# Kernel tuning notes

Hardware: AMD Instinct MI355X
Metric: run time of the kernel (lower is better)

Reference implementation:

```python
import jax, jax.numpy as jnp
import numpy as np

DIM = 2240; HEADS = 20; HD = 112
B = 1; F = 8; H = 16; W = 28; S = F * H * W; ENC = 300
HID = int(3.0 * DIM)  # 6720
EPS_LN = 1e-6; EPS_RMS = 1e-5


def setup_inputs():
    ks = iter(jax.random.split(jax.random.key(0), 64))
    nrm = lambda shape, s=1.0: jax.random.normal(next(ks), shape, jnp.float32) * s
    wsc = 0.02
    inp = dict(
        hidden_states=nrm((B, S, DIM)),
        encoder_hidden_states=nrm((B, ENC, DIM)),
        timestep=nrm((B, 6 * DIM), 0.1),
        freqs_cos=nrm((1, S, 1, HD)),
        freqs_sin=nrm((1, S, 1, HD)),
        scale_shift_table=nrm((6, DIM), 1.0 / np.sqrt(DIM)),
    )
    for p in ("a1", "a2"):
        inp[p + "_qw"] = nrm((DIM, DIM), wsc); inp[p + "_qb"] = jnp.zeros((DIM,), jnp.float32)
        inp[p + "_kw"] = nrm((DIM, DIM), wsc); inp[p + "_kb"] = jnp.zeros((DIM,), jnp.float32)
        inp[p + "_vw"] = nrm((DIM, DIM), wsc); inp[p + "_vb"] = jnp.zeros((DIM,), jnp.float32)
        inp[p + "_nq"] = jnp.ones((DIM,), jnp.float32)
        inp[p + "_nk"] = jnp.ones((DIM,), jnp.float32)
        inp[p + "_ow"] = nrm((DIM, DIM), wsc); inp[p + "_ob"] = jnp.zeros((DIM,), jnp.float32)
    inp["ff_inv_w"] = nrm((1, 1, DIM, 2 * HID), wsc)
    inp["ff_inv_b"] = jnp.zeros((2 * HID,), jnp.float32)
    inp["ff_depth_w"] = nrm((3, 3, 1, 2 * HID), wsc)
    inp["ff_depth_b"] = jnp.zeros((2 * HID,), jnp.float32)
    inp["ff_point_w"] = nrm((1, 1, HID, DIM), wsc)
    inp["ff_temp_w"] = nrm((3, 1, DIM, DIM), wsc)
    inp["frames"] = F; inp["height"] = H; inp["width"] = W
    return inp


def _ln(x):  # LayerNorm, no affine (elementwise_affine=False)
    m = jnp.mean(x, -1, keepdims=True)
    v = jnp.mean((x - m) ** 2, -1, keepdims=True)
    return (x - m) * jax.lax.rsqrt(v + EPS_LN)


def _rms(x, w):  # rms_norm_across_heads on full inner dim
    return x * jax.lax.rsqrt(jnp.mean(x * x, -1, keepdims=True) + EPS_RMS) * w


def _rope(x, cos, sin):  # interleaved rotary as in SanaLinearAttnProcessor3_0
    x1, x2 = x[..., 0::2], x[..., 1::2]
    c, s = cos[..., 0::2], sin[..., 1::2]
    out = jnp.stack([x1 * c - x2 * s, x1 * s + x2 * c], axis=-1)
    return out.reshape(x.shape)


def _conv(x, k, padding, groups=1):
    return jax.lax.conv_general_dilated(
        x, k, (1, 1), padding,
        dimension_numbers=("NHWC", "HWIO", "NHWC"),
        feature_group_count=groups)


def _linear_attn(x, qw, qb, kw, kb, vw, vb, nq, nk, ow, ob, cos, sin):
    b, s, _ = x.shape
    q = jax.nn.relu(_rms(x @ qw + qb, nq)).reshape(b, s, HEADS, HD)
    k = jax.nn.relu(_rms(x @ kw + kb, nk)).reshape(b, s, HEADS, HD)
    v = (x @ vw + vb).reshape(b, s, HEADS, HD)
    qr, kr = _rope(q, cos, sin), _rope(k, cos, sin)
    ksum = jnp.sum(k, axis=1)                             # [b,h,d] (un-rotated)
    denom = jnp.einsum("bhd,bshd->bsh", ksum, q) + 1e-15  # z^{-1}
    scores = jnp.einsum("bshe,bshd->bhed", v, kr)         # [b,h,dv,d]
    out = jnp.einsum("bhed,bshd->bshe", scores, qr) / denom[..., None]
    return out.reshape(b, s, HEADS * HD) @ ow + ob


def _cross_attn(x, enc, qw, qb, kw, kb, vw, vb, nq, nk, ow, ob):
    b, s, _ = x.shape; t = enc.shape[1]
    q = _rms(x @ qw + qb, nq).reshape(b, s, HEADS, HD)
    k = _rms(enc @ kw + kb, nk).reshape(b, t, HEADS, HD)
    v = (enc @ vw + vb).reshape(b, t, HEADS, HD)
    logits = jnp.einsum("bshd,bthd->bhst", q, k) / np.sqrt(HD).astype(np.float32)
    attn = jax.nn.softmax(logits, axis=-1)
    out = jnp.einsum("bhst,bthd->bshd", attn, v).reshape(b, s, HEADS * HD)
    return out @ ow + ob


def _ff(x, inv_w, inv_b, depth_w, depth_b, point_w, temp_w, f, h, w):
    b = x.shape[0]
    y = x.reshape(b * f, h, w, DIM)
    y = jax.nn.silu(_conv(y, inv_w, "SAME") + inv_b)
    y = _conv(y, depth_w, "SAME", groups=2 * HID) + depth_b
    a, g = y[..., :HID], y[..., HID:]
    y = _conv(a * jax.nn.silu(g), point_w, "SAME")        # [bf,h,w,DIM]
    yt = y.reshape(b, f, h * w, DIM)                      # conv over frames axis
    yt = yt + _conv(yt, temp_w, ((1, 1), (0, 0)))
    return yt.reshape(b, f, h, w, DIM)


def reference(hidden_states, encoder_hidden_states, timestep, freqs_cos, freqs_sin,
              scale_shift_table,
              a1_qw, a1_qb, a1_kw, a1_kb, a1_vw, a1_vb, a1_nq, a1_nk, a1_ow, a1_ob,
              a2_qw, a2_qb, a2_kw, a2_kb, a2_vw, a2_vb, a2_nq, a2_nk, a2_ow, a2_ob,
              ff_inv_w, ff_inv_b, ff_depth_w, ff_depth_b, ff_point_w, ff_temp_w,
              frames, height, width):
    b = hidden_states.shape[0]
    mods = scale_shift_table[None] + timestep.reshape(b, 6, DIM)
    sh_msa, sc_msa, g_msa, sh_mlp, sc_mlp, g_mlp = jnp.split(mods, 6, axis=1)
    nh = _ln(hidden_states) * (1 + sc_msa) + sh_msa
    attn = _linear_attn(nh, a1_qw, a1_qb, a1_kw, a1_kb, a1_vw, a1_vb,
                        a1_nq, a1_nk, a1_ow, a1_ob, freqs_cos, freqs_sin)
    x = hidden_states + g_msa * attn
    x = x + _cross_attn(x, encoder_hidden_states, a2_qw, a2_qb, a2_kw, a2_kb,
                        a2_vw, a2_vb, a2_nq, a2_nk, a2_ow, a2_ob)
    nh = _ln(x) * (1 + sc_mlp) + sh_mlp
    ff = _ff(nh.reshape(b, frames, height, width, DIM),
             ff_inv_w, ff_inv_b, ff_depth_w, ff_depth_b, ff_point_w, ff_temp_w,
             frames, height, width)
    x = x + g_mlp * ff.reshape(b, frames * height * width, DIM)
    return x
```

## Files before the change

kernel.cpp:

```cpp
#include <hip/hip_runtime.h>

#define DIMC 2240
#define STOK 3584
#define ENCT 300
#define NH   20
#define HDIM 112
#define HID1 6720
#define HID2 13440
#define DD   (2240*2240)
#define SD   (3584*2240)

typedef short bf16x8 __attribute__((ext_vector_type(8)));
typedef float f32x4  __attribute__((ext_vector_type(4)));

__device__ __forceinline__ unsigned short f2bf(float f){
  unsigned int u = __float_as_uint(f);
  u += 0x7fffu + ((u >> 16) & 1u);
  return (unsigned short)(u >> 16);
}
__device__ __forceinline__ float bf2f(unsigned short h){
  return __uint_as_float(((unsigned int)h) << 16);
}
__device__ __forceinline__ void gl_lds16(const unsigned short* g, unsigned short* l){
  __builtin_amdgcn_global_load_lds(
      (const __attribute__((address_space(1))) unsigned int*)(const void*)g,
      (__attribute__((address_space(3))) unsigned int*)(void*)l, 16, 0, 0);
}

__global__ void cvt_k(const float4* __restrict__ src, ushort4* __restrict__ dst, int n4){
  int i = blockIdx.x*256 + threadIdx.x;
  if (i < n4){
    float4 v = src[i];
    ushort4 o; o.x = f2bf(v.x); o.y = f2bf(v.y); o.z = f2bf(v.z); o.w = f2bf(v.w);
    dst[i] = o;
  }
}

__global__ __launch_bounds__(256) void cvtT3_k(const float* __restrict__ s0,
    const float* __restrict__ s1, const float* __restrict__ s2,
    unsigned short* __restrict__ dst, int rows, int ldsrc, int c0, int nc,
    int ldd, long long dzoff){
  const float* src = (blockIdx.z == 0) ? s0 : ((blockIdx.z == 1) ? s1 : s2);
  unsigned short* d = dst + (size_t)blockIdx.z * (size_t)dzoff;
  __shared__ float tile[32][33];
  const int tx = threadIdx.x & 31, ty = threadIdx.x >> 5;
  const int colBase = blockIdx.x*32;
  #pragma unroll
  for (int i = 0; i < 4; ++i){
    int rr = blockIdx.y*32 + ty + i*8;
    int cc = colBase + tx;
    tile[ty + i*8][tx] = (cc < nc) ? src[(size_t)rr*ldsrc + c0 + cc] : 0.f;
  }
  __syncthreads();
  #pragma unroll
  for (int i = 0; i < 4; ++i){
    int n = colBase + ty + i*8;
    int k = blockIdx.y*32 + tx;
    d[(size_t)n*ldd + k] = f2bf(tile[tx][ty + i*8]);
  }
}

__global__ void zpad_k(unsigned short* __restrict__ m0, unsigned short* __restrict__ m1){
  int i = blockIdx.x*256 + threadIdx.x;
  if (i < 125440){
    reinterpret_cast<uint4*>(m0)[i] = make_uint4(0u,0u,0u,0u);
    reinterpret_cast<uint4*>(m1)[i] = make_uint4(0u,0u,0u,0u);
  }
}

__global__ void pack3_k(float* __restrict__ dst, const float* __restrict__ b0,
    const float* __restrict__ b1, const float* __restrict__ b2, int nslots){
  int i = blockIdx.x*256 + threadIdx.x;
  if (i >= nslots*2304) return;
  int slot = i / 2304, d = i - slot*2304;
  const float* src = (slot == 0) ? b0 : ((slot == 1) ? b1 : b2);
  dst[i] = (d < 2240) ? src[d] : 0.f;
}

__global__ void mods_k(const float* __restrict__ sst, const float* __restrict__ ts, float* __restrict__ mods){
  int i = blockIdx.x*256 + threadIdx.x;
  if (i < 6*DIMC) mods[i] = sst[i] + ts[i];
}

__global__ __launch_bounds__(256) void ln_mod_k(const float* __restrict__ x,
    const float* __restrict__ mods, int shj, int scj, unsigned short* __restrict__ out)
{
  const int s = blockIdx.x;
  const float4* row4 = reinterpret_cast<const float4*>(x + (size_t)s*DIMC);
  const float4* sh4 = reinterpret_cast<const float4*>(mods + shj*DIMC);
  const float4* sc4 = reinterpret_cast<const float4*>(mods + scj*DIMC);
  float sum = 0.f, sq = 0.f;
  for (int o = threadIdx.x; o < 560; o += 256){
    float4 v = row4[o];
    sum += v.x + v.y + v.z + v.w;
    sq  += v.x*v.x + v.y*v.y + v.z*v.z + v.w*v.w;
  }
  #pragma unroll
  for (int o = 32; o; o >>= 1){ sum += __shfl_down(sum, o); sq += __shfl_down(sq, o); }
  __shared__ float sA[4], sB[4];
  int w = threadIdx.x >> 6, l = threadIdx.x & 63;
  if (!l){ sA[w] = sum; sB[w] = sq; }
  __syncthreads();
  sum = sA[0]+sA[1]+sA[2]+sA[3];
  sq  = sB[0]+sB[1]+sB[2]+sB[3];
  float mean = sum * (1.f/DIMC);
  float rs = rsqrtf(sq*(1.f/DIMC) - mean*mean + 1e-6f);
  unsigned short* orow = out + (size_t)s*DIMC;
  for (int o = threadIdx.x; o < 560; o += 256){
    float4 v = row4[o], sc = sc4[o], sh = sh4[o];
    ushort4 r;
    r.x = f2bf((v.x-mean)*rs*(1.f + sc.x) + sh.x);
    r.y = f2bf((v.y-mean)*rs*(1.f + sc.y) + sh.y);
    r.z = f2bf((v.z-mean)*rs*(1.f + sc.z) + sh.z);
    r.w = f2bf((v.w-mean)*rs*(1.f + sc.w) + sh.w);
    *reinterpret_cast<ushort4*>(orow + o*4) = r;
  }
}

template<int RELU, int ROPE>
__global__ __launch_bounds__(256) void rms_bf_k(unsigned short* __restrict__ x, const float* __restrict__ nw,
    const float* __restrict__ cosb, const float* __restrict__ sinb, unsigned short* __restrict__ xr)
{
  const int s = blockIdx.x;
  unsigned short* row = x + (size_t)s*DIMC;
  float sq = 0.f;
  for (int o = threadIdx.x; o < 280; o += 256){
    uint4 v = *reinterpret_cast<const uint4*>(row + o*8);
    unsigned int uu[4] = {v.x, v.y, v.z, v.w};
    #pragma unroll
    for (int j = 0; j < 4; ++j){
      float lo = bf2f((unsigned short)(uu[j] & 0xffffu));
      float hi = bf2f((unsigned short)(uu[j] >> 16));
      sq += lo*lo + hi*hi;
    }
  }
  #pragma unroll
  for (int o = 32; o; o >>= 1) sq += __shfl_down(sq, o);
  __shared__ float sB[4];
  int w = threadIdx.x >> 6, l = threadIdx.x & 63;
  if (!l) sB[w] = sq;
  __syncthreads();
  sq = sB[0]+sB[1]+sB[2]+sB[3];
  float rs = rsqrtf(sq*(1.f/DIMC) + 1e-5f);
  for (int o = threadIdx.x; o < 280; o += 256){
    uint4 v = *reinterpret_cast<const uint4*>(row + o*8);
    unsigned int uu[4] = {v.x, v.y, v.z, v.w};
    float4 n0 = *reinterpret_cast<const float4*>(nw + o*8);
    float4 n1 = *reinterpret_cast<const float4*>(nw + o*8 + 4);
    float nn[8] = {n0.x,n0.y,n0.z,n0.w,n1.x,n1.y,n1.z,n1.w};
    float vals[8];
    #pragma unroll
    for (int j = 0; j < 4; ++j){
      vals[2*j]   = bf2f((unsigned short)(uu[j] & 0xffffu))*rs*nn[2*j];
      vals[2*j+1] = bf2f((unsigned short)(uu[j] >> 16))*rs*nn[2*j+1];
    }
    if constexpr (RELU){
      #pragma unroll
      for (int j = 0; j < 8; ++j) vals[j] = fmaxf(vals[j], 0.f);
    }
    uint4 o1;
    unsigned int* po = &o1.x;
    #pragma unroll
    for (int j = 0; j < 4; ++j)
      po[j] = (unsigned int)f2bf(vals[2*j]) | ((unsigned int)f2bf(vals[2*j+1]) << 16);
    *reinterpret_cast<uint4*>(row + o*8) = o1;
    if constexpr (ROPE){
      int jb = (o*8) % HDIM;
      uint4 o2;
      unsigned int* pr = &o2.x;
      #pragma unroll
      for (int p = 0; p < 4; ++p){
        float c  = cosb[(size_t)s*HDIM + jb + 2*p];
        float sn = sinb[(size_t)s*HDIM + jb + 2*p + 1];
        float r0 = vals[2*p]*c - vals[2*p+1]*sn;
        float r1 = vals[2*p]*sn + vals[2*p+1]*c;
        pr[p] = (unsigned int)f2bf(r0) | ((unsigned int)f2bf(r1) << 16);
      }
      *reinterpret_cast<uint4*>(xr + (size_t)s*DIMC + o*8) = o2;
    }
  }
}

template<int EPI>
__global__ __launch_bounds__(256) void gemm_bt(
  const unsigned short* __restrict__ A, const unsigned short* __restrict__ Bt,
  const float* __restrict__ bias, float* __restrict__ Cf, unsigned short* __restrict__ Cb,
  const float* __restrict__ res, const float* __restrict__ gate,
  int M, int N, int K, int ldc, int PW, int lda, int tcsh)
{
  __shared__ __align__(16) unsigned short Al[128*64];
  __shared__ __align__(16) unsigned short Bl[128*64];
  const int gx = gridDim.x, gy = gridDim.y;
  const int nwg = gx*gy;
  const int orig = blockIdx.y*gx + blockIdx.x;
  const int qq = nwg >> 3, rr = nwg & 7;
  const int xcd = orig & 7, li = orig >> 3;
  const int wg = (xcd < rr ? xcd*(qq+1) : rr*(qq+1) + (xcd-rr)*qq) + li;
  const int ppw = gy*PW;
  const int panel = wg / ppw, rm = wg - panel*ppw;
  const int mrow = rm / PW;
  const int m0 = mrow*128;
  const int n0 = (panel*PW + (rm - mrow*PW))*128;

  const int t = threadIdx.x, lane = t & 63, w = t >> 6;
  const int wr = w >> 1, wc = w & 1;
  const int l16 = lane & 15, lk = lane >> 4;

  const int lr8 = lane >> 3;
  const int sc  = (lane & 7) ^ lr8;
  const unsigned short* Aps[4];
  const unsigned short* Bps[4];
  #pragma unroll
  for (int i = 0; i < 4; ++i){
    int ar = m0 + w*32 + i*8 + lr8;
    int br = n0 + w*32 + i*8 + lr8;
    Aps[i] = A  + (size_t)min(ar, M-1)*lda + sc*8;
    Bps[i] = Bt + (size_t)br*K + sc*8;
  }
  unsigned short* Ad = Al + w*2048;
  unsigned short* Bd = Bl + w*2048;

  f32x4 acc[4][4] = {};
  for (int k0 = 0; k0 < K; k0 += 64){
    size_t aoff;
    if (tcsh){
      int sec = (k0 >= 4480) ? 2 : ((k0 >= 2240) ? 1 : 0);
      aoff = (size_t)(sec*448)*lda + (unsigned)(k0 - sec*2240);
    } else {
      aoff = (size_t)k0;
    }
    __syncthreads();
    #pragma unroll
    for (int i = 0; i < 4; ++i){
      gl_lds16(Aps[i] + aoff, Ad + i*512);
      gl_lds16(Bps[i] + k0,   Bd + i*512);
    }
    __syncthreads();
    #pragma unroll
    for (int kk = 0; kk < 2; ++kk){
      bf16x8 af[4], bfr[4];
      const int chb = (kk*4 + lk) ^ (l16 & 7);
      #pragma unroll
      for (int m = 0; m < 4; ++m)
        af[m] = *reinterpret_cast<const bf16x8*>(Al + (wr*64 + m*16 + l16)*64 + chb*8);
      #pragma unroll
      for (int n = 0; n < 4; ++n)
        bfr[n] = *reinterpret_cast<const bf16x8*>(Bl + (wc*64 + n*16 + l16)*64 + chb*8);
      #pragma unroll
      for (int m = 0; m < 4; ++m)
        #pragma unroll
        for (int n = 0; n < 4; ++n)
          acc[m][n] = __builtin_amdgcn_mfma_f32_16x16x32_bf16(af[m], bfr[n], acc[m][n], 0, 0, 0);
    }
  }

  const int rb = m0 + wr*64 + lk*4;
  const int cb = n0 + wc*64 + l16;
  #pragma unroll
  for (int m = 0; m < 4; ++m){
    #pragma unroll
    for (int r = 0; r < 4; ++r){
      int row = rb + m*16 + r;
      if (row >= M) continue;
      #pragma unroll
      for (int n = 0; n < 4; ++n){
        int col = cb + n*16;
        if (col >= N) continue;
        float v = acc[m][n][r];
        float bv = bias ? bias[col] : 0.f;
        if constexpr (EPI == 6){
          int slot = col / 2304;
          int d = col - slot*2304;
          if (d < 2240)
            Cb[(size_t)slot*ldc + (size_t)row*2240 + d] = f2bf(v + bv);
        } else {
          size_t idx = (size_t)row*ldc + col;
          if constexpr (EPI == 0){ Cf[idx] = v + bv; }
          else if constexpr (EPI == 1){ float u = v + bv; Cb[idx] = f2bf(u / (1.f + __expf(-u))); }
          else if constexpr (EPI == 2){ Cb[idx] = f2bf(v + bv); }
          else if constexpr (EPI == 3){ float u = res[idx] + gate[col]*(v + bv); Cf[idx] = u; Cb[idx] = f2bf(u); }
          else if constexpr (EPI == 4){ Cf[idx] = res[idx] + v + bv; }
          else if constexpr (EPI == 7){ Cf[idx] = res[idx] + gate[col]*(bf2f(Cb[idx]) + v); }
          else { Cf[idx] += v; }
        }
      }
    }
  }
}

__global__ void colsum_k(const unsigned short* __restrict__ k, float* __restrict__ kpart){
  int d = blockIdx.x*256 + threadIdx.x;
  if (d >= DIMC) return;
  int ch = blockIdx.y, s0 = ch*128;
  float acc = 0.f;
  for (int s = s0; s < s0+128; ++s) acc += bf2f(k[(size_t)s*DIMC + d]);
  kpart[(size_t)ch*DIMC + d] = acc;
}
__global__ void ksumred_k(const float* __restrict__ kpart, float* __restrict__ ksum){
  int d = blockIdx.x*256 + threadIdx.x;
  if (d >= DIMC) return;
  float a = 0.f;
  for (int c = 0; c < 28; ++c) a += kpart[(size_t)c*DIMC + d];
  ksum[d] = a;
}
__global__ __launch_bounds__(256) void denom_k(const unsigned short* __restrict__ q,
    const float* __restrict__ ksum, float* __restrict__ denom)
{
  int s = blockIdx.x; int w = threadIdx.x >> 6, l = threadIdx.x & 63;
  for (int h = w; h < NH; h += 4){
    const unsigned short* qb = q + (size_t)s*DIMC + h*HDIM;
    const float* kb = ksum + h*HDIM;
    float v = bf2f(qb[l])*kb[l];
    if (l < 48) v += bf2f(qb[64+l])*kb[64+l];
    #pragma unroll
    for (int o = 32; o; o >>= 1) v += __shfl_down(v, o);
    if (!l) denom[s*NH + h] = v + 1e-15f;
  }
}

#define SLSC 136
__device__ __forceinline__ int sc_idx(int e, int s){
  return e*SLSC + (s ^ (((e >> 3) & 7) << 3));
}
__global__ __launch_bounds__(256) void scores_k(const unsigned short* __restrict__ v,
    const unsigned short* __restrict__ kr, float* __restrict__ part)
{
  const int h = blockIdx.x, ch = blockIdx.y;
  __shared__ __align__(16) unsigned short Vt[112*SLSC];
  __shared__ __align__(16) unsigned short Kt[112*SLSC];
  const int t = threadIdx.x, lane = t & 63, w = t >> 6;
  const int l16 = lane & 15, lk = lane >> 4;
  const int sbase = ch*128;

  for (int p = t; p < 1792; p += 256){
    int s = p / 14, oc = (p % 14) * 8;
    bf16x8 vv = *reinterpret_cast<const bf16x8*>(v  + (size_t)(sbase+s)*DIMC + h*HDIM + oc);
    bf16x8 kk = *reinterpret_cast<const bf16x8*>(kr + (size_t)(sbase+s)*DIMC + h*HDIM + oc);
    #pragma unroll
    for (int j = 0; j < 8; ++j){
      Vt[sc_idx(oc+j, s)] = (unsigned short)vv[j];
      Kt[sc_idx(oc+j, s)] = (unsigned short)kk[j];
    }
  }
  __syncthreads();

  f32x4 acc[2][7] = {};
  #pragma unroll
  for (int ks = 0; ks < 4; ++ks){
    const int sf = ks*32 + lk*8;
    bf16x8 bfrg[7];
    #pragma unroll
    for (int nt = 0; nt < 7; ++nt){
      int d = nt*16 + l16;
      bfrg[nt] = *reinterpret_cast<const bf16x8*>(&Kt[d*SLSC + (sf ^ (((d >> 3) & 7) << 3))]);
    }
    #pragma unroll
    for (int mi = 0; mi < 2; ++mi){
      int mt = w + mi*4;
      if (mt < 7){
        int e = mt*16 + l16;
        bf16x8 afrg = *reinterpret_cast<const bf16x8*>(&Vt[e*SLSC + (sf ^ (((e >> 3) & 7) << 3))]);
        #pragma unroll
        for (int nt = 0; nt < 7; ++nt)
          acc[mi][nt] = __builtin_amdgcn_mfma_f32_16x16x32_bf16(afrg, bfrg[nt], acc[mi][nt], 0, 0, 0);
      }
    }
  }

  float* pout = part + ((size_t)ch*NH + h)*12544;
  #pragma unroll
  for (int mi = 0; mi < 2; ++mi){
    int mt = w + mi*4;
    if (mt >= 7) continue;
    #pragma unroll
    for (int nt = 0; nt < 7; ++nt)
      #pragma unroll
      for (int r = 0; r < 4; ++r)
        pout[(size_t)(mt*16 + lk*4 + r)*HDIM + nt*16 + l16] = acc[mi][nt][r];
  }
}
__global__ void scred_k(const float* __restrict__ part, unsigned short* __restrict__ sc){
  int i = blockIdx.x*256 + threadIdx.x;
  if (i >= NH*HDIM*HDIM) return;
  float a = 0.f;
  #pragma unroll
  for (int c = 0; c < 28; ++c) a += part[(size_t)c*(NH*HDIM*HDIM) + i];
  sc[i] = f2bf(a);
}

__global__ __launch_bounds__(256) void linout_k(const unsigned short* __restrict__ qr,
    const unsigned short* __restrict__ scores, const float* __restrict__ denom,
    unsigned short* __restrict__ out)
{
  const int h = blockIdx.y;
  const int t = threadIdx.x, lane = t & 63, w = t >> 6;
  const int l16 = lane & 15, lk = lane >> 4;
  const int s0 = blockIdx.x*64 + w*16;
  const unsigned short* qrow = qr + (size_t)(s0 + l16)*DIMC + h*HDIM;
  const unsigned short* sb = scores + (size_t)h*12544;
  f32x4 acc[7] = {};
  #pragma unroll
  for (int ks = 0; ks < 4; ++ks){
    int d0 = ks*32 + lk*8;
    bf16x8 a = {};
    if (d0 < HDIM) a = *reinterpret_cast<const bf16x8*>(qrow + d0);
    #pragma unroll
    for (int nt = 0; nt < 7; ++nt){
      bf16x8 b = {};
      if (d0 < HDIM) b = *reinterpret_cast<const bf16x8*>(sb + (size_t)(nt*16 + l16)*HDIM + d0);
      acc[nt] = __builtin_amdgcn_mfma_f32_16x16x32_bf16(a, b, acc[nt], 0, 0, 0);
    }
  }
  #pragma unroll
  for (int r = 0; r < 4; ++r){
    int s = s0 + lk*4 + r;
    float dn = 1.f / denom[(size_t)s*NH + h];
    #pragma unroll
    for (int nt = 0; nt < 7; ++nt)
      out[(size_t)s*DIMC + h*HDIM + nt*16 + l16] = f2bf(acc[nt][r]*dn);
  }
}

__global__ __launch_bounds__(256) void xattn_k(
    const unsigned short* __restrict__ q,
    const unsigned short* __restrict__ k2,
    const unsigned short* __restrict__ v2,
    unsigned short* __restrict__ outb)
{
  const int h = blockIdx.y;
  const int w = threadIdx.x >> 6, lane = threadIdx.x & 63;
  const int l16 = lane & 15, lk = lane >> 4;
  const float scale = 0.09449111825230679f;

  __shared__ __align__(16) unsigned short Kl[64][136];
  __shared__ __align__(16) unsigned short Vl[112][72];
  __shared__ __align__(16) unsigned short Pl[4][16][72];

  bf16x8 qf[4];
  const unsigned short* qbase = q + (size_t)(blockIdx.x*64 + w*16 + l16)*DIMC + h*HDIM;
  #pragma unroll
  for (int c = 0; c < 4; ++c){
    int d0 = c*32 + lk*8;
    bf16x8 z = {};
    qf[c] = (d0 < HDIM) ? *reinterpret_cast<const bf16x8*>(qbase + d0) : z;
  }

  f32x4 lg[5][4] = {};
  #pragma unroll
  for (int c = 0; c < 5; ++c){
    const int kbase = c*64;
    const int nk = (c == 4) ? (ENCT - 256) : 64;
    __syncthreads();
    #pragma unroll
    for (int it = 0; it < 4; ++it){
      int li = it*256 + threadIdx.x;
      int key = li >> 4, d0 = (li & 15) << 3;
      uint4 val = make_uint4(0u,0u,0u,0u);
      if (key < nk && d0 < HDIM)
        val = *reinterpret_cast<const uint4*>(k2 + (size_t)(kbase+key)*DIMC + h*HDIM + d0);
      *reinterpret_cast<uint4*>(&Kl[key][d0]) = val;
    }
    __syncthreads();
    #pragma unroll
    for (int nt = 0; nt < 4; ++nt){
      #pragma unroll
      for (int ks = 0; ks < 4; ++ks){
        bf16x8 kf = *reinterpret_cast<const bf16x8*>(&Kl[nt*16 + l16][ks*32 + lk*8]);
        lg[c][nt] = __builtin_amdgcn_mfma_f32_16x16x32_bf16(qf[ks], kf, lg[c][nt], 0, 0, 0);
      }
    }
  }

  float mx[4] = {-3e38f, -3e38f, -3e38f, -3e38f};
  #pragma unroll
  for (int c = 0; c < 5; ++c)
    #pragma unroll
    for (int nt = 0; nt < 4; ++nt){
      bool valid = (c*64 + nt*16 + l16) < ENCT;
      #pragma unroll
      for (int r = 0; r < 4; ++r){
        float v = valid ? lg[c][nt][r]*scale : -3e38f;
        lg[c][nt][r] = v;
        mx[r] = fmaxf(mx[r], v);
      }
    }
  #pragma unroll
  for (int o = 1; o < 16; o <<= 1)
    #pragma unroll
    for (int r = 0; r < 4; ++r) mx[r] = fmaxf(mx[r], __shfl_xor(mx[r], o));
  float sm[4] = {0.f, 0.f, 0.f, 0.f};
  #pragma unroll
  for (int c = 0; c < 5; ++c)
    #pragma unroll
    for (int nt = 0; nt < 4; ++nt)
      #pragma unroll
      for (int r = 0; r < 4; ++r){
        float e = __expf(lg[c][nt][r] - mx[r]);
        lg[c][nt][r] = e;
        sm[r] += e;
      }
  #pragma unroll
  for (int o = 1; o < 16; o <<= 1)
    #pragma unroll
    for (int r = 0; r < 4; ++r) sm[r] += __shfl_xor(sm[r], o);
  float inv[4];
  #pragma unroll
  for (int r = 0; r < 4; ++r) inv[r] = 1.f / sm[r];

  f32x4 oacc[7] = {};
  #pragma unroll
  for (int c = 0; c < 5; ++c){
    const int kbase = c*64;
    const int nk = (c == 4) ? (ENCT - 256) : 64;
    __syncthreads();
    #pragma unroll
    for (int it = 0; it < 4; ++it){
      int li = it*256 + threadIdx.x;
      if (li < 896){
        int key = li/14, d0 = (li%14)*8;
        if (key < nk){
          bf16x8 vv = *reinterpret_cast<const bf16x8*>(v2 + (size_t)(kbase+key)*DIMC + h*HDIM + d0);
          #pragma unroll
          for (int j = 0; j < 8; ++j) Vl[d0+j][key] = (unsigned short)vv[j];
        } else {
          #pragma unroll
          for (int j = 0; j < 8; ++j) Vl[d0+j][key] = 0;
        }
      }
    }
    #pragma unroll
    for (int nt = 0; nt < 4; ++nt)
      #pragma unroll
      for (int r = 0; r < 4; ++r)
        Pl[w][lk*4 + r][nt*16 + l16] = f2bf(lg[c][nt][r]);
    __syncthreads();
    #pragma unroll
    for (int ks = 0; ks < 2; ++ks){
      bf16x8 pf = *reinterpret_cast<const bf16x8*>(&Pl[w][l16][ks*32 + lk*8]);
      #pragma unroll
      for (int n = 0; n < 7; ++n){
        bf16x8 vf = *reinterpret_cast<const bf16x8*>(&Vl[n*16 + l16][ks*32 + lk*8]);
        oacc[n] = __builtin_amdgcn_mfma_f32_16x16x32_bf16(pf, vf, oacc[n], 0, 0, 0);
      }
    }
  }

  const int orow = blockIdx.x*64 + w*16 + lk*4;
  #pragma unroll
  for (int n = 0; n < 7; ++n)
    #pragma unroll
    for (int r = 0; r < 4; ++r)
      outb[(size_t)(orow + r)*DIMC + h*HDIM + n*16 + l16] = f2bf(oacc[n][r]*inv[r]);
}

__global__ __launch_bounds__(256) void dw_k(const unsigned short* __restrict__ y1,
    const float* __restrict__ dw, const float* __restrict__ db, unsigned short* __restrict__ y2)
{
  int c = (blockIdx.y*256 + threadIdx.x)*2;
  if (c >= HID1) return;
  int bx = blockIdx.x;
  int xq = bx % 7;
  int yt = (bx / 7) & 3;
  int f  = bx / 28;
  int x0 = xq*4, y0 = yt*4;

  float wa[9][2], wg[9][2];
  #pragma unroll
  for (int tp = 0; tp < 9; ++tp){
    float2 va = *reinterpret_cast<const float2*>(dw + tp*HID2 + c);
    float2 vg = *reinterpret_cast<const float2*>(dw + tp*HID2 + c + HID1);
    wa[tp][0] = va.x; wa[tp][1] = va.y;
    wg[tp][0] = vg.x; wg[tp][1] = vg.y;
  }
  float2 ba = *reinterpret_cast<const float2*>(db + c);
  float2 bg = *reinterpret_cast<const float2*>(db + c + HID1);
  float a[4][4][2], g[4][4][2];
  #pragma unroll
  for (int r = 0; r < 4; ++r)
    #pragma unroll
    for (int cc = 0; cc < 4; ++cc){
      a[r][cc][0] = ba.x; a[r][cc][1] = ba.y;
      g[r][cc][0] = bg.x; g[r][cc][1] = bg.y;
    }

  #pragma unroll
  for (int dy6 = 0; dy6 < 6; ++dy6){
    int y = y0 - 1 + dy6;
    if ((unsigned)y >= 16u) continue;
    #pragma unroll
    for (int dxc = 0; dxc < 6; ++dxc){
      int x = x0 - 1 + dxc;
      if ((unsigned)x >= 28u) continue;
      size_t base = ((size_t)(f*16 + y)*28 + x)*HID2;
      unsigned int a01 = *reinterpret_cast<const unsigned int*>(y1 + base + c);
      unsigned int g01 = *reinterpret_cast<const unsigned int*>(y1 + base + c + HID1);
      float fa0 = bf2f((unsigned short)(a01 & 0xffffu));
      float fa1 = bf2f((unsigned short)(a01 >> 16));
      float fg0 = bf2f((unsigned short)(g01 & 0xffffu));
      float fg1 = bf2f((unsigned short)(g01 >> 16));
      #pragma unroll
      for (int r = 0; r < 4; ++r){
        int kdy = dy6 - r;
        if (kdy < 0 || kdy > 2) continue;
        #pragma unroll
        for (int cc = 0; cc < 4; ++cc){
          int kdx = dxc - cc;
          if (kdx < 0 || kdx > 2) continue;
          int tp = kdy*3 + kdx;
          a[r][cc][0] += fa0*wa[tp][0]; a[r][cc][1] += fa1*wa[tp][1];
          g[r][cc][0] += fg0*wg[tp][0]; g[r][cc][1] += fg1*wg[tp][1];
        }
      }
    }
  }
  #pragma unroll
  for (int r = 0; r < 4; ++r)
    #pragma unroll
    for (int cc = 0; cc < 4; ++cc){
      float s0 = g[r][cc][0] / (1.f + __expf(-g[r][cc][0]));
      float s1 = g[r][cc][1] / (1.f + __expf(-g[r][cc][1]));
      int pos = (f*16 + y0 + r)*28 + x0 + cc;
      unsigned int o = (unsigned int)f2bf(a[r][cc][0]*s0) | ((unsigned int)f2bf(a[r][cc][1]*s1) << 16);
      *reinterpret_cast<unsigned int*>(y2 + (size_t)pos*HID1 + c) = o;
    }
}

extern "C" void kernel_launch(void* const* d_in, const int* in_sizes, int n_in,
                              void* d_out, int out_size, void* d_ws, size_t ws_size,
                              hipStream_t stream)
{
  const float* hid   = (const float*)d_in[0];
  const float* enc   = (const float*)d_in[1];
  const float* tstep = (const float*)d_in[2];
  const float* fcos  = (const float*)d_in[3];
  const float* fsin  = (const float*)d_in[4];
  const float* sst   = (const float*)d_in[5];
  const float *a1_qw=(const float*)d_in[6],  *a1_qb=(const float*)d_in[7];
  const float *a1_kw=(const float*)d_in[8],  *a1_kb=(const float*)d_in[9];
  const float *a1_vw=(const float*)d_in[10], *a1_vb=(const float*)d_in[11];
  const float *a1_nq=(const float*)d_in[12], *a1_nk=(const float*)d_in[13];
  const float *a1_ow=(const float*)d_in[14], *a1_ob=(const float*)d_in[15];
  const float *a2_qw=(const float*)d_in[16], *a2_qb=(const float*)d_in[17];
  const float *a2_kw=(const float*)d_in[18], *a2_kb=(const float*)d_in[19];
  const float *a2_vw=(const float*)d_in[20], *a2_vb=(const float*)d_in[21];
  const float *a2_nq=(const float*)d_in[22], *a2_nk=(const float*)d_in[23];
  const float *a2_ow=(const float*)d_in[24], *a2_ob=(const float*)d_in[25];
  const float *ff_inv_w=(const float*)d_in[26], *ff_inv_b=(const float*)d_in[27];
  const float *ff_dw=(const float*)d_in[28], *ff_db=(const float*)d_in[29];
  const float *ff_pw=(const float*)d_in[30];
  const float *ff_tw=(const float*)d_in[31];
  float* out = (float*)d_out;

  const size_t SLOTB = (size_t)SD*2;
  char* ws = (char*)d_ws;
  size_t off = 0;
  auto alloc = [&](size_t n){ void* p = ws + off; off += (n + 255) & ~(size_t)255; return p; };

  char* P = (char*)alloc(6*SLOTB);
  float* x1    = (float*)alloc((size_t)SD*4);
  unsigned short* nh2b = (unsigned short*)alloc(SLOTB);
  float* x2    = (float*)alloc((size_t)SD*4);
  unsigned short* k2b = (unsigned short*)alloc((size_t)ENCT*DIMC*2);
  unsigned short* v2b = (unsigned short*)alloc((size_t)ENCT*DIMC*2);
  unsigned short* encb = (unsigned short*)alloc((size_t)ENCT*DIMC*2);
  float* modsb = (float*)alloc(6*DIMC*4);
  float* ksum  = (float*)alloc(DIMC*4);
  float* kpart = (float*)alloc((size_t)28*DIMC*4);
  float* denom = (float*)alloc((size_t)STOK*NH*4);
  unsigned short* scorb = (unsigned short*)alloc((size_t)NH*HDIM*HDIM*2);
  float* bias3 = (float*)alloc(3*2304*4);
  unsigned short* Wbig = (unsigned short*)alloc((size_t)6912*DIMC*2);

  unsigned short* P0 = (unsigned short*)P;
  unsigned short* P1 = (unsigned short*)(P + 1*SLOTB);
  unsigned short* P2 = (unsigned short*)(P + 2*SLOTB);
  unsigned short* P3 = (unsigned short*)(P + 3*SLOTB);
  unsigned short* P4 = (unsigned short*)(P + 4*SLOTB);
  unsigned short* P5 = (unsigned short*)(P + 5*SLOTB);
  unsigned short* nhb = P0;
  unsigned short* y1b = P0;
  unsigned short* y2b = (unsigned short*)x1;
  unsigned short* y3pad = P0;
  unsigned short* y3  = y3pad + (size_t)448*DIMC;
  float* spart = (float*)P1;

  auto cvt = [&](const float* s, unsigned short* d, size_t n){
    int n4 = (int)(n/4);
    cvt_k<<<dim3((n4+255)/256), 256, 0, stream>>>((const float4*)s, (ushort4*)d, n4);
  };
  auto cvtT3 = [&](const float* s0, const float* s1, const float* s2, unsigned short* d,
                   int rows, int ldsrc, int c0, int nc, int ncPad, int ldd, long long dzoff, int nz){
    cvtT3_k<<<dim3(ncPad/32, rows/32, nz), 256, 0, stream>>>(s0, s1, s2, d, rows, ldsrc, c0, nc, ldd, dzoff);
  };
  auto gemm_grid = [&](int M, int Npad){ return dim3(Npad/128, (M+127)/128); };
  const long long WSLOT = (long long)2304*DIMC;

  mods_k<<<dim3((6*DIMC+255)/256), 256, 0, stream>>>(sst, tstep, modsb);
  cvt(enc, encb, (size_t)ENCT*DIMC);

  ln_mod_k<<<dim3(STOK), 256, 0, stream>>>(hid, modsb, 0, 1, nhb);
  pack3_k<<<dim3((3*2304+255)/256), 256, 0, stream>>>(bias3, a1_qb, a1_kb, a1_vb, 3);
  cvtT3(a1_qw, a1_kw, a1_vw, Wbig, DIMC, DIMC, 0, DIMC, 2304, DIMC, WSLOT, 3);
  gemm_bt<6><<<gemm_grid(STOK, 6912), 256, 0, stream>>>(nhb, Wbig, bias3, nullptr, P1,
                                                        nullptr, nullptr, STOK, 6912, DIMC, SD, 6, DIMC, 0);
  rms_bf_k<1,1><<<dim3(STOK), 256, 0, stream>>>(P1, a1_nq, fcos, fsin, P4);
  rms_bf_k<1,1><<<dim3(STOK), 256, 0, stream>>>(P2, a1_nk, fcos, fsin, P5);
  colsum_k<<<dim3(9, 28), 256, 0, stream>>>(P2, kpart);
  ksumred_k<<<dim3(9), 256, 0, stream>>>(kpart, ksum);
  denom_k<<<dim3(STOK), 256, 0, stream>>>(P1, ksum, denom);
  scores_k<<<dim3(NH, 28), 256, 0, stream>>>(P3, P5, spart);
  scred_k<<<dim3((NH*HDIM*HDIM+255)/256), 256, 0, stream>>>(spart, scorb);
  linout_k<<<dim3(STOK/64, NH), 256, 0, stream>>>(P4, scorb, denom, P1);
  dim3 gMN = gemm_grid(STOK, 2304);
  cvtT3(a1_ow, a2_qw, a2_ow, Wbig, DIMC, DIMC, 0, DIMC, 2304, DIMC, WSLOT, 3);
  gemm_bt<3><<<gMN, 256, 0, stream>>>(P1, Wbig, a1_ob, x1, P2, hid, modsb + 2*DIMC, STOK, DIMC, DIMC, DIMC, 6, DIMC, 0);

  gemm_bt<2><<<gMN, 256, 0, stream>>>(P2, Wbig + WSLOT, a2_qb, nullptr, P3, nullptr, nullptr, STOK, DIMC, DIMC, DIMC, 6, DIMC, 0);
  pack3_k<<<dim3((2*2304+255)/256), 256, 0, stream>>>(bias3, a2_kb, a2_vb, a2_vb, 2);
  cvtT3(a2_kw, a2_vw, a2_vw, Wbig, DIMC, DIMC, 0, DIMC, 2304, DIMC, WSLOT, 2);
  gemm_bt<6><<<gemm_grid(ENCT, 4608), 256, 0, stream>>>(encb, Wbig, bias3, nullptr, k2b,
                                                        nullptr, nullptr, ENCT, 4608, DIMC, ENCT*DIMC, 6, DIMC, 0);
  rms_bf_k<0,0><<<dim3(STOK), 256, 0, stream>>>(P3, a2_nq, nullptr, nullptr, nullptr);
  rms_bf_k<0,0><<<dim3(ENCT), 256, 0, stream>>>(k2b, a2_nk, nullptr, nullptr, nullptr);
  xattn_k<<<dim3(STOK/64, NH), 256, 0, stream>>>(P3, k2b, v2b, P4);
  gemm_bt<4><<<gMN, 256, 0, stream>>>(P4, Wbig + 2*WSLOT, a2_ob, x2, nullptr, x1, nullptr, STOK, DIMC, DIMC, DIMC, 6, DIMC, 0);

  ln_mod_k<<<dim3(STOK), 256, 0, stream>>>(x2, modsb, 3, 4, nh2b);
  for (int q = 0; q < 2; ++q){
    int c0 = q*6720;
    cvtT3(ff_inv_w, ff_inv_w, ff_inv_w, Wbig, DIMC, HID2, c0, 6720, 6912, DIMC, 0, 1);
    gemm_bt<1><<<gemm_grid(STOK, 6912), 256, 0, stream>>>(nh2b, Wbig, ff_inv_b + c0, nullptr, y1b + c0,
                                                          nullptr, nullptr, STOK, 6720, DIMC, HID2, 6, DIMC, 0);
  }
  dw_k<<<dim3(224, 14), 256, 0, stream>>>(y1b, ff_dw, ff_db, y2b);
  zpad_k<<<dim3(490), 256, 0, stream>>>(y3pad, y3pad + (size_t)(448 + STOK)*DIMC);
  cvtT3(ff_pw, ff_pw, ff_pw, Wbig, HID1, DIMC, 0, DIMC, 2304, HID1, 0, 1);
  gemm_bt<2><<<gMN, 256, 0, stream>>>(y2b, Wbig, nullptr, nullptr, y3,
                                      nullptr, nullptr, STOK, DIMC, HID1, DIMC, 2, HID1, 0);
  cvtT3(ff_tw, ff_tw + (size_t)DD, ff_tw + (size_t)2*DD, Wbig,
        DIMC, DIMC, 0, DIMC, 2304, 6720, 2240LL, 3);
  gemm_bt<7><<<gMN, 256, 0, stream>>>(y3pad, Wbig, nullptr, out, y3, x2, modsb + 5*DIMC,
                                      STOK, DIMC, 6720, DIMC, 2, DIMC, 1);
}
```

Baseline: 1.358 ms.

## Merge small prep kernels and keep residual stream in bf16

```diff
diff --git a/kernel.cpp b/kernel.cpp
--- a/kernel.cpp
+++ b/kernel.cpp
@@ -27,12 +27,22 @@
       (__attribute__((address_space(3))) unsigned int*)(void*)l, 16, 0, 0);
 }
 
-__global__ void cvt_k(const float4* __restrict__ src, ushort4* __restrict__ dst, int n4){
+__global__ void prep_k(const float* __restrict__ sst, const float* __restrict__ ts,
+    float* __restrict__ mods,
+    const float* __restrict__ b0, const float* __restrict__ b1, const float* __restrict__ b2,
+    const float* __restrict__ b3, const float* __restrict__ b4, float* __restrict__ bias5,
+    const float4* __restrict__ encs, ushort4* __restrict__ encd){
   int i = blockIdx.x*256 + threadIdx.x;
-  if (i < n4){
-    float4 v = src[i];
+  if (i < 168000){
+    float4 v = encs[i];
     ushort4 o; o.x = f2bf(v.x); o.y = f2bf(v.y); o.z = f2bf(v.z); o.w = f2bf(v.w);
-    dst[i] = o;
+    encd[i] = o;
+  }
+  if (i < 6*DIMC) mods[i] = sst[i] + ts[i];
+  if (i < 5*2304){
+    int slot = i / 2304, d = i - slot*2304;
+    const float* s = (slot==0)?b0 : (slot==1)?b1 : (slot==2)?b2 : (slot==3)?b3 : b4;
+    bias5[i] = (d < 2240) ? s[d] : 0.f;
   }
 }
 
@@ -66,20 +76,6 @@
     reinterpret_cast<uint4*>(m0)[i] = make_uint4(0u,0u,0u,0u);
     reinterpret_cast<uint4*>(m1)[i] = make_uint4(0u,0u,0u,0u);
   }
-}
-
-__global__ void pack3_k(float* __restrict__ dst, const float* __restrict__ b0,
-    const float* __restrict__ b1, const float* __restrict__ b2, int nslots){
-  int i = blockIdx.x*256 + threadIdx.x;
-  if (i >= nslots*2304) return;
-  int slot = i / 2304, d = i - slot*2304;
-  const float* src = (slot == 0) ? b0 : ((slot == 1) ? b1 : b2);
-  dst[i] = (d < 2240) ? src[d] : 0.f;
-}
-
-__global__ void mods_k(const float* __restrict__ sst, const float* __restrict__ ts, float* __restrict__ mods){
-  int i = blockIdx.x*256 + threadIdx.x;
-  if (i < 6*DIMC) mods[i] = sst[i] + ts[i];
 }
 
 __global__ __launch_bounds__(256) void ln_mod_k(const float* __restrict__ x,
@@ -117,12 +113,60 @@
   }
 }
 
-template<int RELU, int ROPE>
-__global__ __launch_bounds__(256) void rms_bf_k(unsigned short* __restrict__ x, const float* __restrict__ nw,
-    const float* __restrict__ cosb, const float* __restrict__ sinb, unsigned short* __restrict__ xr)
+__global__ __launch_bounds__(256) void ln_mod_bf_k(const unsigned short* __restrict__ x,
+    const float* __restrict__ mods, int shj, int scj, unsigned short* __restrict__ out)
 {
   const int s = blockIdx.x;
-  unsigned short* row = x + (size_t)s*DIMC;
+  const unsigned short* row = x + (size_t)s*DIMC;
+  float sum = 0.f, sq = 0.f;
+  for (int o = threadIdx.x; o < 280; o += 256){
+    uint4 v = *reinterpret_cast<const uint4*>(row + o*8);
+    unsigned int uu[4] = {v.x, v.y, v.z, v.w};
+    #pragma unroll
+    for (int j = 0; j < 4; ++j){
+      float lo = bf2f((unsigned short)(uu[j] & 0xffffu));
+      float hi = bf2f((unsigned short)(uu[j] >> 16));
+      sum += lo + hi; sq += lo*lo + hi*hi;
+    }
+  }
+  #pragma unroll
+  for (int o = 32; o; o >>= 1){ sum += __shfl_down(sum, o); sq += __shfl_down(sq, o); }
+  __shared__ float sA[4], sB[4];
+  int w = threadIdx.x >> 6, l = threadIdx.x & 63;
+  if (!l){ sA[w] = sum; sB[w] = sq; }
+  __syncthreads();
+  sum = sA[0]+sA[1]+sA[2]+sA[3];
+  sq  = sB[0]+sB[1]+sB[2]+sB[3];
+  float mean = sum * (1.f/DIMC);
+  float rs = rsqrtf(sq*(1.f/DIMC) - mean*mean + 1e-6f);
+  unsigned short* orow = out + (size_t)s*DIMC;
+  const float* sh = mods + shj*DIMC;
+  const float* sc = mods + scj*DIMC;
+  for (int o = threadIdx.x; o < 280; o += 256){
+    uint4 v = *reinterpret_cast<const uint4*>(row + o*8);
+    unsigned int uu[4] = {v.x, v.y, v.z, v.w};
+    uint4 ov;
+    unsigned int* po = &ov.x;
+    #pragma unroll
+    for (int j = 0; j < 4; ++j){
+      int d0 = o*8 + 2*j;
+      float lo = (bf2f((unsigned short)(uu[j] & 0xffffu)) - mean)*rs*(1.f + sc[d0])   + sh[d0];
+      float hi = (bf2f((unsigned short)(uu[j] >> 16))     - mean)*rs*(1.f + sc[d0+1]) + sh[d0+1];
+      po[j] = (unsigned int)f2bf(lo) | ((unsigned int)f2bf(hi) << 16);
+    }
+    *reinterpret_cast<uint4*>(orow + o*8) = ov;
+  }
+}
+
+__global__ __launch_bounds__(256) void rmsqk_k(unsigned short* __restrict__ qx,
+    unsigned short* __restrict__ kx, const float* __restrict__ nq, const float* __restrict__ nk,
+    const float* __restrict__ cosb, const float* __restrict__ sinb,
+    unsigned short* __restrict__ qr, unsigned short* __restrict__ kr)
+{
+  const int s = blockIdx.x;
+  unsigned short* row = (blockIdx.y ? kx : qx) + (size_t)s*DIMC;
+  const float* nw = blockIdx.y ? nk : nq;
+  unsigned short* xr = (blockIdx.y ? kr : qr) + (size_t)s*DIMC;
   float sq = 0.f;
   for (int o = threadIdx.x; o < 280; o += 256){
     uint4 v = *reinterpret_cast<const uint4*>(row + o*8);
@@ -151,12 +195,8 @@
     float vals[8];
     #pragma unroll
     for (int j = 0; j < 4; ++j){
-      vals[2*j]   = bf2f((unsigned short)(uu[j] & 0xffffu))*rs*nn[2*j];
-      vals[2*j+1] = bf2f((unsigned short)(uu[j] >> 16))*rs*nn[2*j+1];
-    }
-    if constexpr (RELU){
-      #pragma unroll
-      for (int j = 0; j < 8; ++j) vals[j] = fmaxf(vals[j], 0.f);
+      vals[2*j]   = fmaxf(bf2f((unsigned short)(uu[j] & 0xffffu))*rs*nn[2*j],   0.f);
+      vals[2*j+1] = fmaxf(bf2f((unsigned short)(uu[j] >> 16))*rs*nn[2*j+1], 0.f);
     }
     uint4 o1;
     unsigned int* po = &o1.x;
@@ -164,20 +204,62 @@
     for (int j = 0; j < 4; ++j)
       po[j] = (unsigned int)f2bf(vals[2*j]) | ((unsigned int)f2bf(vals[2*j+1]) << 16);
     *reinterpret_cast<uint4*>(row + o*8) = o1;
-    if constexpr (ROPE){
-      int jb = (o*8) % HDIM;
-      uint4 o2;
-      unsigned int* pr = &o2.x;
-      #pragma unroll
-      for (int p = 0; p < 4; ++p){
-        float c  = cosb[(size_t)s*HDIM + jb + 2*p];
-        float sn = sinb[(size_t)s*HDIM + jb + 2*p + 1];
-        float r0 = vals[2*p]*c - vals[2*p+1]*sn;
-        float r1 = vals[2*p]*sn + vals[2*p+1]*c;
-        pr[p] = (unsigned int)f2bf(r0) | ((unsigned int)f2bf(r1) << 16);
-      }
-      *reinterpret_cast<uint4*>(xr + (size_t)s*DIMC + o*8) = o2;
-    }
+    int jb = (o*8) % HDIM;
+    uint4 o2;
+    unsigned int* pr = &o2.x;
+    #pragma unroll
+    for (int p = 0; p < 4; ++p){
+      float c  = cosb[(size_t)s*HDIM + jb + 2*p];
+      float sn = sinb[(size_t)s*HDIM + jb + 2*p + 1];
+      float r0 = vals[2*p]*c - vals[2*p+1]*sn;
+      float r1 = vals[2*p]*sn + vals[2*p+1]*c;
+      pr[p] = (unsigned int)f2bf(r0) | ((unsigned int)f2bf(r1) << 16);
+    }
+    *reinterpret_cast<uint4*>(xr + o*8) = o2;
+  }
+}
+
+__global__ __launch_bounds__(256) void rmsnn_k(unsigned short* __restrict__ xa,
+    const float* __restrict__ na, unsigned short* __restrict__ xb, const float* __restrict__ nb)
+{
+  int s = blockIdx.x;
+  unsigned short* row; const float* nw;
+  if (s < STOK){ row = xa + (size_t)s*DIMC; nw = na; }
+  else         { row = xb + (size_t)(s - STOK)*DIMC; nw = nb; }
+  float sq = 0.f;
+  for (int o = threadIdx.x; o < 280; o += 256){
+    uint4 v = *reinterpret_cast<const uint4*>(row + o*8);
+    unsigned int uu[4] = {v.x, v.y, v.z, v.w};
+    #pragma unroll
+    for (int j = 0; j < 4; ++j){
+      float lo = bf2f((unsigned short)(uu[j] & 0xffffu));
+      float hi = bf2f((unsigned short)(uu[j] >> 16));
+      sq += lo*lo + hi*hi;
+    }
+  }
+  #pragma unroll
+  for (int o = 32; o; o >>= 1) sq += __shfl_down(sq, o);
+  __shared__ float sB[4];
+  int w = threadIdx.x >> 6, l = threadIdx.x & 63;
+  if (!l) sB[w] = sq;
+  __syncthreads();
+  sq = sB[0]+sB[1]+sB[2]+sB[3];
+  float rs = rsqrtf(sq*(1.f/DIMC) + 1e-5f);
+  for (int o = threadIdx.x; o < 280; o += 256){
+    uint4 v = *reinterpret_cast<const uint4*>(row + o*8);
+    unsigned int uu[4] = {v.x, v.y, v.z, v.w};
+    float4 n0 = *reinterpret_cast<const float4*>(nw + o*8);
+    float4 n1 = *reinterpret_cast<const float4*>(nw + o*8 + 4);
+    float nn[8] = {n0.x,n0.y,n0.z,n0.w,n1.x,n1.y,n1.z,n1.w};
+    uint4 o1;
+    unsigned int* po = &o1.x;
+    #pragma unroll
+    for (int j = 0; j < 4; ++j){
+      float lo = bf2f((unsigned short)(uu[j] & 0xffffu))*rs*nn[2*j];
+      float hi = bf2f((unsigned short)(uu[j] >> 16))*rs*nn[2*j+1];
+      po[j] = (unsigned int)f2bf(lo) | ((unsigned int)f2bf(hi) << 16);
+    }
+    *reinterpret_cast<uint4*>(row + o*8) = o1;
   }
 }
 
@@ -278,9 +360,15 @@
           if constexpr (EPI == 0){ Cf[idx] = v + bv; }
           else if constexpr (EPI == 1){ float u = v + bv; Cb[idx] = f2bf(u / (1.f + __expf(-u))); }
           else if constexpr (EPI == 2){ Cb[idx] = f2bf(v + bv); }
-          else if constexpr (EPI == 3){ float u = res[idx] + gate[col]*(v + bv); Cf[idx] = u; Cb[idx] = f2bf(u); }
-          else if constexpr (EPI == 4){ Cf[idx] = res[idx] + v + bv; }
-          else if constexpr (EPI == 7){ Cf[idx] = res[idx] + gate[col]*(bf2f(Cb[idx]) + v); }
+          else if constexpr (EPI == 3){ float u = res[idx] + gate[col]*(v + bv); Cb[idx] = f2bf(u); }
+          else if constexpr (EPI == 7){
+            const unsigned short* resb = (const unsigned short*)(const void*)res;
+            Cf[idx] = bf2f(resb[idx]) + gate[col]*(bf2f(Cb[idx]) + v);
+          }
+          else if constexpr (EPI == 8){
+            const unsigned short* resb = (const unsigned short*)(const void*)res;
+            Cb[idx] = f2bf(bf2f(resb[idx]) + v + bv);
+          }
           else { Cf[idx] += v; }
         }
       }
@@ -668,7 +756,7 @@
   float* kpart = (float*)alloc((size_t)28*DIMC*4);
   float* denom = (float*)alloc((size_t)STOK*NH*4);
   unsigned short* scorb = (unsigned short*)alloc((size_t)NH*HDIM*HDIM*2);
-  float* bias3 = (float*)alloc(3*2304*4);
+  float* bias5 = (float*)alloc(5*2304*4);
   unsigned short* Wbig = (unsigned short*)alloc((size_t)6912*DIMC*2);
 
   unsigned short* P0 = (unsigned short*)P;
@@ -682,12 +770,9 @@
   unsigned short* y2b = (unsigned short*)x1;
   unsigned short* y3pad = P0;
   unsigned short* y3  = y3pad + (size_t)448*DIMC;
+  unsigned short* x2b = (unsigned short*)x2;
   float* spart = (float*)P1;
 
-  auto cvt = [&](const float* s, unsigned short* d, size_t n){
-    int n4 = (int)(n/4);
-    cvt_k<<<dim3((n4+255)/256), 256, 0, stream>>>((const float4*)s, (ushort4*)d, n4);
-  };
   auto cvtT3 = [&](const float* s0, const float* s1, const float* s2, unsigned short* d,
                    int rows, int ldsrc, int c0, int nc, int ncPad, int ldd, long long dzoff, int nz){
     cvtT3_k<<<dim3(ncPad/32, rows/32, nz), 256, 0, stream>>>(s0, s1, s2, d, rows, ldsrc, c0, nc, ldd, dzoff);
@@ -695,16 +780,14 @@
   auto gemm_grid = [&](int M, int Npad){ return dim3(Npad/128, (M+127)/128); };
   const long long WSLOT = (long long)2304*DIMC;
 
-  mods_k<<<dim3((6*DIMC+255)/256), 256, 0, stream>>>(sst, tstep, modsb);
-  cvt(enc, encb, (size_t)ENCT*DIMC);
+  prep_k<<<dim3(657), 256, 0, stream>>>(sst, tstep, modsb,
+      a1_qb, a1_kb, a1_vb, a2_kb, a2_vb, bias5, (const float4*)enc, (ushort4*)encb);
 
   ln_mod_k<<<dim3(STOK), 256, 0, stream>>>(hid, modsb, 0, 1, nhb);
-  pack3_k<<<dim3((3*2304+255)/256), 256, 0, stream>>>(bias3, a1_qb, a1_kb, a1_vb, 3);
   cvtT3(a1_qw, a1_kw, a1_vw, Wbig, DIMC, DIMC, 0, DIMC, 2304, DIMC, WSLOT, 3);
-  gemm_bt<6><<<gemm_grid(STOK, 6912), 256, 0, stream>>>(nhb, Wbig, bias3, nullptr, P1,
+  gemm_bt<6><<<gemm_grid(STOK, 6912), 256, 0, stream>>>(nhb, Wbig, bias5, nullptr, P1,
                                                         nullptr, nullptr, STOK, 6912, DIMC, SD, 6, DIMC, 0);
-  rms_bf_k<1,1><<<dim3(STOK), 256, 0, stream>>>(P1, a1_nq, fcos, fsin, P4);
-  rms_bf_k<1,1><<<dim3(STOK), 256, 0, stream>>>(P2, a1_nk, fcos, fsin, P5);
+  rmsqk_k<<<dim3(STOK, 2), 256, 0, stream>>>(P1, P2, a1_nq, a1_nk, fcos, fsin, P4, P5);
   colsum_k<<<dim3(9, 28), 256, 0, stream>>>(P2, kpart);
   ksumred_k<<<dim3(9), 256, 0, stream>>>(kpart, ksum);
   denom_k<<<dim3(STOK), 256, 0, stream>>>(P1, ksum, denom);
@@ -713,19 +796,18 @@
   linout_k<<<dim3(STOK/64, NH), 256, 0, stream>>>(P4, scorb, denom, P1);
   dim3 gMN = gemm_grid(STOK, 2304);
   cvtT3(a1_ow, a2_qw, a2_ow, Wbig, DIMC, DIMC, 0, DIMC, 2304, DIMC, WSLOT, 3);
-  gemm_bt<3><<<gMN, 256, 0, stream>>>(P1, Wbig, a1_ob, x1, P2, hid, modsb + 2*DIMC, STOK, DIMC, DIMC, DIMC, 6, DIMC, 0);
+  gemm_bt<3><<<gMN, 256, 0, stream>>>(P1, Wbig, a1_ob, nullptr, P2, hid, modsb + 2*DIMC, STOK, DIMC, DIMC, DIMC, 6, DIMC, 0);
 
   gemm_bt<2><<<gMN, 256, 0, stream>>>(P2, Wbig + WSLOT, a2_qb, nullptr, P3, nullptr, nullptr, STOK, DIMC, DIMC, DIMC, 6, DIMC, 0);
-  pack3_k<<<dim3((2*2304+255)/256), 256, 0, stream>>>(bias3, a2_kb, a2_vb, a2_vb, 2);
   cvtT3(a2_kw, a2_vw, a2_vw, Wbig, DIMC, DIMC, 0, DIMC, 2304, DIMC, WSLOT, 2);
-  gemm_bt<6><<<gemm_grid(ENCT, 4608), 256, 0, stream>>>(encb, Wbig, bias3, nullptr, k2b,
+  gemm_bt<6><<<gemm_grid(ENCT, 4608), 256, 0, stream>>>(encb, Wbig, bias5 + 3*2304, nullptr, k2b,
                                                         nullptr, nullptr, ENCT, 4608, DIMC, ENCT*DIMC, 6, DIMC, 0);
-  rms_bf_k<0,0><<<dim3(STOK), 256, 0, stream>>>(P3, a2_nq, nullptr, nullptr, nullptr);
-  rms_bf_k<0,0><<<dim3(ENCT), 256, 0, stream>>>(k2b, a2_nk, nullptr, nullptr, nullptr);
+  rmsnn_k<<<dim3(STOK + ENCT), 256, 0, stream>>>(P3, a2_nq, k2b, a2_nk);
   xattn_k<<<dim3(STOK/64, NH), 256, 0, stream>>>(P3, k2b, v2b, P4);
-  gemm_bt<4><<<gMN, 256, 0, stream>>>(P4, Wbig + 2*WSLOT, a2_ob, x2, nullptr, x1, nullptr, STOK, DIMC, DIMC, DIMC, 6, DIMC, 0);
-
-  ln_mod_k<<<dim3(STOK), 256, 0, stream>>>(x2, modsb, 3, 4, nh2b);
+  gemm_bt<8><<<gMN, 256, 0, stream>>>(P4, Wbig + 2*WSLOT, a2_ob, nullptr, x2b,
+                                      (const float*)(const void*)P2, nullptr, STOK, DIMC, DIMC, DIMC, 6, DIMC, 0);
+
+  ln_mod_bf_k<<<dim3(STOK), 256, 0, stream>>>(x2b, modsb, 3, 4, nh2b);
   for (int q = 0; q < 2; ++q){
     int c0 = q*6720;
     cvtT3(ff_inv_w, ff_inv_w, ff_inv_w, Wbig, DIMC, HID2, c0, 6720, 6912, DIMC, 0, 1);
@@ -739,6 +821,7 @@
                                       nullptr, nullptr, STOK, DIMC, HID1, DIMC, 2, HID1, 0);
   cvtT3(ff_tw, ff_tw + (size_t)DD, ff_tw + (size_t)2*DD, Wbig,
         DIMC, DIMC, 0, DIMC, 2304, 6720, 2240LL, 3);
-  gemm_bt<7><<<gMN, 256, 0, stream>>>(y3pad, Wbig, nullptr, out, y3, x2, modsb + 5*DIMC,
+  gemm_bt<7><<<gMN, 256, 0, stream>>>(y3pad, Wbig, nullptr, out, y3,
+                                      (const float*)(const void*)x2b, modsb + 5*DIMC,
                                       STOK, DIMC, 6720, DIMC, 2, DIMC, 1);
 }
```

New measurement: 1.332 ms. About the same (-1.9%).
